# Kernel tuning notes

Hardware: AMD Instinct MI355X
Metric: run time of the kernel (lower is better)

Reference implementation:

```python
import jax, jax.numpy as jnp
import numpy as np

NEG_SLOPE = 0.2


def gat_layer(x, adj, W, a_src, a_dst):
    # x: (C, in_dim), adj: (C, C) 0/1, W: (in_dim, H*D), a_src/a_dst: (H, D)
    C = x.shape[0]
    H, D = a_src.shape
    h = (x @ W).reshape(C, H, D)            # (C, H, D)
    hh = jnp.transpose(h, (1, 0, 2))        # (H, C, D)
    asrc = jnp.einsum('hcd,hd->hc', hh, a_src)  # (H, C)
    adst = jnp.einsum('hcd,hd->hc', hh, a_dst)  # (H, C)
    e = asrc[:, :, None] + adst[:, None, :]     # (H, C, C)
    e = jax.nn.leaky_relu(e, NEG_SLOPE)
    e = jnp.where(adj[None, :, :] == 0, -jnp.inf, e)
    attn = jax.nn.softmax(e, axis=-1)           # (H, C, C)
    out = jnp.einsum('hij,hjd->hid', attn, hh)  # (H, C, D)
    return jnp.transpose(out, (1, 0, 2)).reshape(C, H * D)


def setup_inputs() -> dict:
    key = jax.random.key(0)
    ks = jax.random.split(key, 12)
    B, doc_dim = 1024, 768
    C, label_dim = 4096, 768
    hidden, H = 512, 4
    D = hidden // H  # 128

    doc_x = jax.random.normal(ks[0], (B, doc_dim), dtype=jnp.float32)
    label_init = jax.random.normal(ks[1], (C, label_dim), dtype=jnp.float32)
    adj = jax.random.randint(ks[2], (C, C), 0, 2, dtype=jnp.int32)
    adj = adj.at[jnp.arange(C), jnp.arange(C)].set(1)  # self-loops

    def xavier(k, shape):
        fan_in, fan_out = shape[0], shape[1]
        lim = jnp.sqrt(6.0 / (fan_in + fan_out)).astype(jnp.float32)
        return jax.random.uniform(k, shape, jnp.float32, -lim, lim)

    W1 = xavier(ks[3], (label_dim, hidden))
    a_src1 = xavier(ks[4], (H, D))
    a_dst1 = xavier(ks[5], (H, D))
    W2 = xavier(ks[6], (hidden, hidden))
    a_src2 = xavier(ks[7], (H, D))
    a_dst2 = xavier(ks[8], (H, D))
    Wd = xavier(ks[9], (doc_dim, hidden))
    bd = jnp.zeros((hidden,), jnp.float32)
    return {"doc_x": doc_x, "label_init": label_init, "adj": adj,
            "W1": W1, "a_src1": a_src1, "a_dst1": a_dst1,
            "W2": W2, "a_src2": a_src2, "a_dst2": a_dst2,
            "Wd": Wd, "bd": bd}


def reference(doc_x, label_init, adj, W1, a_src1, a_dst1, W2, a_src2, a_dst2, Wd, bd):
    # doc_proj (dropout = identity in eval)
    doc_h = jax.nn.relu(doc_x @ Wd + bd)            # (B, hidden)
    # label encoder: GAT -> ELU -> GAT
    h = gat_layer(label_init, adj, W1, a_src1, a_dst1)
    h = jax.nn.elu(h)
    label_h = gat_layer(h, adj, W2, a_src2, a_dst2)  # (C, hidden)
    logits = doc_h @ label_h.T                      # (B, C)
    return logits
```

## Files before the change

### kernel.cpp

```cpp
#include <hip/hip_runtime.h>
#include <hip/hip_bf16.h>
#include <math.h>

#define BDOCS   1024
#define CNODES  4096
#define INDIM   768
#define HID     512
#define NHEAD   4
#define HDIM    128
#define NEG_SLOPE 0.2f

#define KSPLIT  8
#define JPER    (CNODES / KSPLIT)
#define NCH     (JPER / 32)

typedef __attribute__((ext_vector_type(8))) short short8;
typedef __attribute__((ext_vector_type(4))) float f32x4;

__device__ __forceinline__ float lrelu(float x) { return x > 0.f ? x : NEG_SLOPE * x; }

__device__ __forceinline__ short f2bf(float f) {
    union { float f; unsigned u; } v; v.f = f;
    unsigned r = (v.u + 0x7fff + ((v.u >> 16) & 1)) >> 16;
    return (short)r;
}
__device__ __forceinline__ float bf2f(short s) {
    union { float f; unsigned u; } v; v.u = ((unsigned)(unsigned short)s) << 16;
    return v.f;
}
__device__ __forceinline__ unsigned pk2(float a, float b) {
    union { float f; unsigned u; } x, y; x.f = a; y.f = b;
    unsigned lo = (x.u + 0x7fff + ((x.u >> 16) & 1)) >> 16;
    unsigned hi = (y.u + 0x7fff + ((y.u >> 16) & 1)) >> 16;
    return lo | (hi << 16);
}
__device__ __forceinline__ short hup(float f) {
    union { float f; unsigned u; } v; v.f = f;
    return (short)((v.u + 0x8000) >> 16);
}
__device__ __forceinline__ unsigned encf(float x) {
    union { float f; unsigned u; } v; v.f = x;
    return (v.u & 0x80000000u) ? ~v.u : (v.u | 0x80000000u);
}
__device__ __forceinline__ float decf(unsigned u) {
    union { float f; unsigned u; } v;
    v.u = (u & 0x80000000u) ? (u ^ 0x80000000u) : ~u;
    return v.f;
}

__device__ void frag_T_dev(const float* __restrict__ src, short* __restrict__ dst,
                           int N, int K, int jc, int nq, float (*tile)[132])
{
    const int t  = threadIdx.x;
    const int KC = K >> 5;
#pragma unroll
    for (int it = 0; it < 16; it++) {
        const int e = it * 256 + t;
        const int j = e >> 7, n = e & 127;
        tile[j][n] = src[(size_t)(jc * 32 + j) * N + nq * 128 + n];
    }
    __syncthreads();
#pragma unroll
    for (int s = 0; s < 2; s++) {
        const int item = s * 256 + t;
        const int nbl = item >> 6, lane = item & 63;
        const int nr = lane & 15, kq = lane >> 4;
        short8 v;
#pragma unroll
        for (int jr = 0; jr < 8; jr++)
            v[jr] = f2bf(tile[kq * 8 + jr][nbl * 16 + nr]);
        *(short8*)&dst[((size_t)((nq * 8 + nbl) * KC + jc) * 64 + lane) * 8] = v;
    }
}

__device__ void frag_A_dev(const float* __restrict__ src, short* __restrict__ dst,
                           int C, int rb, int cq, float (*tile)[132])
{
    const int t  = threadIdx.x;
    const int KC = C >> 5;
#pragma unroll
    for (int it = 0; it < 8; it++) {
        const int e = it * 256 + t;
        const int r = e >> 7, c = e & 127;
        tile[r][c] = src[(size_t)(rb * 16 + r) * C + cq * 128 + c];
    }
    __syncthreads();
    const int kcl = t >> 6, lane = t & 63;
    const int m = lane & 15, kq = lane >> 4;
    short8 v8;
#pragma unroll
    for (int j = 0; j < 8; j++) v8[j] = f2bf(tile[m][kcl * 32 + kq * 8 + j]);
    *(short8*)&dst[((size_t)(rb * KC + cq * 4 + kcl) * 64 + lane) * 8] = v8;
}

#define PREP_BLOCKS (65536 + 96 + 96 + 64 + 384 + 1536)
__global__ __launch_bounds__(256)
void prep_all(const int* __restrict__ adj, unsigned long long* __restrict__ adjb64,
              const float* __restrict__ Wd, short* __restrict__ Wdf,
              const float* __restrict__ W1, short* __restrict__ W1f,
              const float* __restrict__ W2, short* __restrict__ W2f,
              const float* __restrict__ doc_x, short* __restrict__ dxf,
              const float* __restrict__ label_init, short* __restrict__ lif,
              unsigned* __restrict__ MhEnc)
{
    __shared__ float tile[32][132];
    int b = blockIdx.x;
    if (b < 65536) {
        if (b == 0 && threadIdx.x < 8) MhEnc[threadIdx.x] = 0u;
        const int t    = threadIdx.x;
        const int gw   = b * 4 + (t >> 6);
        const int lane = t & 63;
        const int i  = gw >> 6;
        const int j0 = (gw & 63) * 64;
        const int a  = adj[(size_t)i * CNODES + j0 + lane];
        const unsigned long long msk = __ballot(a != 0);
        if (lane == 0) adjb64[(size_t)i * 64 + (j0 >> 6)] = msk;
        return;
    }
    b -= 65536;
    if (b < 96)  { frag_T_dev(Wd, Wdf, HID, INDIM, b % 24, b / 24, tile); return; }
    b -= 96;
    if (b < 96)  { frag_T_dev(W1, W1f, HID, INDIM, b % 24, b / 24, tile); return; }
    b -= 96;
    if (b < 64)  { frag_T_dev(W2, W2f, HID, HID, b % 16, b / 16, tile); return; }
    b -= 64;
    if (b < 384) { frag_A_dev(doc_x, dxf, INDIM, b % 64, b / 64, tile); return; }
    b -= 384;
    frag_A_dev(label_init, lif, INDIM, b % 256, b / 256, tile);
}

template <int KC>
__global__ __launch_bounds__(64)
void gemm_hpre(const short* __restrict__ Af, const short* __restrict__ Bf,
               const float* __restrict__ a_src, const float* __restrict__ a_dst,
               short* __restrict__ hbTf, float* __restrict__ asrc, float* __restrict__ adst,
               unsigned* __restrict__ MhEnc)
{
    __shared__ __align__(16) short tileT[128][24];
    const int lane = threadIdx.x;
    const int mb   = blockIdx.x;
    const int nq   = blockIdx.y;
    const int i0   = mb * 16;

    f32x4 acc[8];
#pragma unroll
    for (int c = 0; c < 8; c++) acc[c] = (f32x4){0.f, 0.f, 0.f, 0.f};

    const short* ap = Af + (size_t)mb * KC * 512 + lane * 8;
    const short* bp = Bf + (size_t)(nq * 8) * KC * 512 + lane * 8;

#pragma unroll 2
    for (int kc = 0; kc < KC; kc++) {
        short8 a = *(const short8*)(ap + (size_t)kc * 512);
#pragma unroll
        for (int c = 0; c < 8; c++) {
            short8 bf = *(const short8*)(bp + ((size_t)c * KC + kc) * 512);
            acc[c] = __builtin_amdgcn_mfma_f32_16x16x32_bf16(a, bf, acc[c], 0, 0, 0);
        }
    }

    const int col = lane & 15, q4 = lane >> 4;

#pragma unroll
    for (int c = 0; c < 8; c++) {
        uint2 u;
        u.x = pk2(acc[c][0], acc[c][1]);
        u.y = pk2(acc[c][2], acc[c][3]);
        *(uint2*)&tileT[c * 16 + col][q4 * 4] = u;
    }
    __syncthreads();
    {
        const int jc = mb >> 1, khalf = mb & 1;
        const int nr = lane & 15, kq = lane >> 4;
        if ((kq >> 1) == khalf) {
#pragma unroll
            for (int nbl = 0; nbl < 8; nbl++) {
                short8 v = *(const short8*)&tileT[nbl * 16 + nr][(kq & 1) * 8];
                *(short8*)&hbTf[(((size_t)(nq * 8 + nbl) * (CNODES / 32) + jc) * 64 + lane) * 8] = v;
            }
        }
    }

    float ssrc[4] = {}, sdst[4] = {};
#pragma unroll
    for (int c = 0; c < 8; c++) {
        const float vs = a_src[nq * 128 + c * 16 + col];
        const float vd = a_dst[nq * 128 + c * 16 + col];
#pragma unroll
        for (int r = 0; r < 4; r++) {
            ssrc[r] += acc[c][r] * vs;
            sdst[r] += acc[c][r] * vd;
        }
    }
#pragma unroll
    for (int mask = 1; mask <= 8; mask <<= 1)
#pragma unroll
        for (int r = 0; r < 4; r++) {
            ssrc[r] += __shfl_xor(ssrc[r], mask);
            sdst[r] += __shfl_xor(sdst[r], mask);
        }
    if (col == 0) {
#pragma unroll
        for (int r = 0; r < 4; r++) {
            const int row = i0 + q4 * 4 + r;
            asrc[nq * CNODES + row] = ssrc[r];
            adst[nq * CNODES + row] = sdst[r];
        }
    }
    float wmax = fmaxf(fmaxf(sdst[0], sdst[1]), fmaxf(sdst[2], sdst[3]));
    wmax = fmaxf(wmax, __shfl_xor(wmax, 16));
    wmax = fmaxf(wmax, __shfl_xor(wmax, 32));
    if (lane == 0) atomicMax(MhEnc + nq, encf(wmax));
}

template <int KC>
__global__ __launch_bounds__(64)
void gemm_doc(const short* __restrict__ Af, const short* __restrict__ Bf,
              const float* __restrict__ bias, short* __restrict__ dhf)
{
    __shared__ __align__(16) short tile[16][64];
    const int lane = threadIdx.x;
    const int mb = blockIdx.x;
    const int ng = blockIdx.y;

    f32x4 acc[4];
#pragma unroll
    for (int c = 0; c < 4; c++) acc[c] = (f32x4){0.f, 0.f, 0.f, 0.f};

    const short* ap = Af + (size_t)mb * KC * 512 + lane * 8;
    const short* bp = Bf + (size_t)(ng * 4) * KC * 512 + lane * 8;

#pragma unroll 2
    for (int kc = 0; kc < KC; kc++) {
        short8 a = *(const short8*)(ap + (size_t)kc * 512);
#pragma unroll
        for (int c = 0; c < 4; c++) {
            short8 bf = *(const short8*)(bp + ((size_t)c * KC + kc) * 512);
            acc[c] = __builtin_amdgcn_mfma_f32_16x16x32_bf16(a, bf, acc[c], 0, 0, 0);
        }
    }

    const int col = lane & 15, q4 = lane >> 4;
#pragma unroll
    for (int c = 0; c < 4; c++)
#pragma unroll
        for (int r = 0; r < 4; r++) {
            float v = fmaxf(acc[c][r] + bias[ng * 64 + c * 16 + col], 0.f);
            tile[q4 * 4 + r][c * 16 + col] = f2bf(v);
        }
    __syncthreads();
    const int m = lane & 15, kq = lane >> 4;
#pragma unroll
    for (int kcl = 0; kcl < 2; kcl++) {
        short8 v = *(const short8*)&tile[m][kcl * 32 + kq * 8];
        *(short8*)&dhf[(((size_t)mb * 16 + ng * 2 + kcl) * 64 + lane) * 8] = v;
    }
}

template <int KC>
__global__ __launch_bounds__(64)
void gemm_frag(const short* __restrict__ Af, const short* __restrict__ Bf,
               float* __restrict__ Cmat, int N)
{
    const int lane = threadIdx.x;
    const int mb0  = blockIdx.x * 2;
    const int nq   = blockIdx.y;

    f32x4 acc[2][8];
#pragma unroll
    for (int f = 0; f < 2; f++)
#pragma unroll
        for (int c = 0; c < 8; c++) acc[f][c] = (f32x4){0.f, 0.f, 0.f, 0.f};

    const short* ap0 = Af + (size_t)mb0 * KC * 512 + lane * 8;
    const short* ap1 = ap0 + (size_t)KC * 512;
    const short* bp  = Bf + (size_t)(nq * 8) * KC * 512 + lane * 8;

#pragma unroll 2
    for (int kc = 0; kc < KC; kc++) {
        short8 a0 = *(const short8*)(ap0 + (size_t)kc * 512);
        short8 a1 = *(const short8*)(ap1 + (size_t)kc * 512);
#pragma unroll
        for (int c = 0; c < 8; c++) {
            short8 bf = *(const short8*)(bp + ((size_t)c * KC + kc) * 512);
            acc[0][c] = __builtin_amdgcn_mfma_f32_16x16x32_bf16(a0, bf, acc[0][c], 0, 0, 0);
            acc[1][c] = __builtin_amdgcn_mfma_f32_16x16x32_bf16(a1, bf, acc[1][c], 0, 0, 0);
        }
    }

    const int col = lane & 15, q4 = lane >> 4;
#pragma unroll
    for (int f = 0; f < 2; f++)
#pragma unroll
        for (int c = 0; c < 8; c++)
#pragma unroll
            for (int r = 0; r < 4; r++) {
                const int row = (mb0 + f) * 16 + q4 * 4 + r;
                Cmat[(size_t)row * N + nq * 128 + c * 16 + col] = acc[f][c][r];
            }
}

__global__ __launch_bounds__(512, 2)
void attn_pv(const short* __restrict__ hbTf,
             const unsigned int* __restrict__ adjb,
             const float* __restrict__ asrc, const float* __restrict__ adst,
             const unsigned* __restrict__ MhEnc,
             short* __restrict__ part, float* __restrict__ lpart)
{
    __shared__ __align__(16) float E1s[NHEAD][512];
    __shared__ __align__(16) float E2s[NHEAD][512];
    __shared__ __align__(16) short tileO[32][520];

    const int t    = threadIdx.x;
    const int ww   = t >> 6;
    const int w    = ww & 3;
    const int f2   = ww >> 2;
    const int lane = t & 63;
    const int m    = lane & 15;
    const int kq   = lane >> 4;
    const int i0   = blockIdx.x * 64;
    const int iw   = i0 + f2 * 32;
    const int ks   = blockIdx.y;
    const int js   = ks * JPER;

    {
        const int j = js + t;
#pragma unroll
        for (int h = 0; h < NHEAD; h++) {
            const float d = adst[h * CNODES + j] - decf(MhEnc[h]);
            E1s[h][t] = __expf(d);
            E2s[h][t] = __expf(0.2f * d);
        }
    }

    const float mh  = decf(MhEnc[w]);
    const float as0 = asrc[w * CNODES + iw + m];
    const float as1 = asrc[w * CNODES + iw + 16 + m];
    const float mr0 = lrelu(as0 + mh), mr1 = lrelu(as1 + mh);
    const float A10 = __expf(as0 + mh - mr0),          A11 = __expf(as1 + mh - mr1);
    const float A20 = __expf(0.2f * (as0 + mh) - mr0), A21 = __expf(0.2f * (as1 + mh) - mr1);
    const float T00 = __expf(-as0 - mh),               T01 = __expf(-as1 - mh);

    f32x4 acc[2][8], accO[2];
#pragma unroll
    for (int f = 0; f < 2; f++) {
        accO[f] = (f32x4){0.f, 0.f, 0.f, 0.f};
#pragma unroll
        for (int c = 0; c < 8; c++) acc[f][c] = (f32x4){0.f, 0.f, 0.f, 0.f};
    }
    short8 ones;
#pragma unroll
    for (int q = 0; q < 8; q++) ones[q] = (short)0x3F80;

    const unsigned int* ar0 = adjb + (size_t)(iw + m) * 128 + ks * NCH;
    const unsigned int* ar1 = adjb + (size_t)(iw + 16 + m) * 128 + ks * NCH;

    __syncthreads();

#pragma unroll 2
    for (int ch = 0; ch < NCH; ch++) {
        const int jl = ch * 32;
        const unsigned int aw0 = ar0[ch] >> (kq * 8);
        const unsigned int aw1 = ar1[ch] >> (kq * 8);
        const float4 x0 = *(const float4*)&E1s[w][jl + kq * 8];
        const float4 x1 = *(const float4*)&E1s[w][jl + kq * 8 + 4];
        const float4 y0 = *(const float4*)&E2s[w][jl + kq * 8];
        const float4 y1 = *(const float4*)&E2s[w][jl + kq * 8 + 4];
        const float e1v[8] = {x0.x, x0.y, x0.z, x0.w, x1.x, x1.y, x1.z, x1.w};
        const float e2v[8] = {y0.x, y0.y, y0.z, y0.w, y1.x, y1.y, y1.z, y1.w};

        short8 a0, a1;
#pragma unroll
        for (int q = 0; q < 8; q++) {
            const float e1 = e1v[q], e2 = e2v[q];
            const bool c0 = e1 > T00, c1 = e1 > T01;
            float w0 = (c0 ? A10 : A20) * (c0 ? e1 : e2);
            float w1 = (c1 ? A11 : A21) * (c1 ? e1 : e2);
            w0 = ((aw0 >> q) & 1u) ? w0 : 0.f;
            w1 = ((aw1 >> q) & 1u) ? w1 : 0.f;
            a0[q] = hup(w0);
            a1[q] = hup(w1);
        }

        const short* bbase = hbTf + (((size_t)(w * 8) * 128 + ((js + jl) >> 5)) * 64 + lane) * 8;
#pragma unroll
        for (int c = 0; c < 8; c++) {
            short8 bf = *(const short8*)(bbase + (size_t)c * 128 * 64 * 8);
            acc[0][c] = __builtin_amdgcn_mfma_f32_16x16x32_bf16(a0, bf, acc[0][c], 0, 0, 0);
            acc[1][c] = __builtin_amdgcn_mfma_f32_16x16x32_bf16(a1, bf, acc[1][c], 0, 0, 0);
        }
        accO[0] = __builtin_amdgcn_mfma_f32_16x16x32_bf16(a0, ones, accO[0], 0, 0, 0);
        accO[1] = __builtin_amdgcn_mfma_f32_16x16x32_bf16(a1, ones, accO[1], 0, 0, 0);
    }

    if (m == 0) {
#pragma unroll
        for (int f = 0; f < 2; f++)
#pragma unroll
            for (int r = 0; r < 4; r++)
                lpart[((size_t)ks * NHEAD + w) * CNODES + iw + f * 16 + kq * 4 + r] = accO[f][r];
    }

    short* pS = part + (size_t)ks * CNODES * HID;
    for (int half = 0; half < 2; half++) {
        __syncthreads();
        if (f2 == half) {
#pragma unroll
            for (int f = 0; f < 2; f++)
#pragma unroll
                for (int c = 0; c < 8; c++)
#pragma unroll
                    for (int r = 0; r < 4; r++)
                        tileO[f * 16 + kq * 4 + r][w * 128 + c * 16 + m] = f2bf(acc[f][c][r]);
        }
        __syncthreads();
#pragma unroll
        for (int it = 0; it < 4; it++) {
            const int u   = it * 512 + t;
            const int row = u >> 6, un = u & 63;
            uint4 v = *(const uint4*)&tileO[row][un * 8];
            *(uint4*)&pS[(size_t)(i0 + half * 32 + row) * HID + un * 8] = v;
        }
    }
}

template <bool ELU>
__global__ __launch_bounds__(256)
void reduce_norm_frag(const short* __restrict__ part, const float* __restrict__ lpart,
                      short* __restrict__ dst)
{
    const int t = threadIdx.x;
    const int W = blockIdx.x * 4 + (t >> 6);
    const int lane = t & 63;
    const int rb = W >> 4, kc = W & 15;
    const int m = lane & 15, kq = lane >> 4;
    const int i = rb * 16 + m;
    const int n0 = kc * 32 + kq * 8;
    const int h = kc >> 2;

    float v[8] = {};
    float l = 0.f;
#pragma unroll
    for (int s = 0; s < KSPLIT; s++) {
        const uint4 raw = *(const uint4*)&part[(size_t)s * CNODES * HID + (size_t)i * HID + n0];
        const unsigned rr[4] = {raw.x, raw.y, raw.z, raw.w};
#pragma unroll
        for (int q = 0; q < 4; q++) {
            v[q * 2]     += bf2f((short)(rr[q] & 0xffff));
            v[q * 2 + 1] += bf2f((short)(rr[q] >> 16));
        }
        l += lpart[((size_t)s * NHEAD + h) * CNODES + i];
    }
    const float inv = 1.0f / l;
    short8 o;
#pragma unroll
    for (int q = 0; q < 8; q++) {
        float x = v[q] * inv;
        if (ELU) x = x > 0.f ? x : (__expf(x) - 1.f);
        o[q] = f2bf(x);
    }
    *(short8*)&dst[((size_t)(rb * 16 + kc) * 64 + lane) * 8] = o;
}

extern "C" void kernel_launch(void* const* d_in, const int* in_sizes, int n_in,
                              void* d_out, int out_size, void* d_ws, size_t ws_size,
                              hipStream_t stream)
{
    const float* doc_x      = (const float*)d_in[0];
    const float* label_init = (const float*)d_in[1];
    const int*   adj        = (const int*)d_in[2];
    const float* W1         = (const float*)d_in[3];
    const float* a_src1     = (const float*)d_in[4];
    const float* a_dst1     = (const float*)d_in[5];
    const float* W2         = (const float*)d_in[6];
    const float* a_src2     = (const float*)d_in[7];
    const float* a_dst2     = (const float*)d_in[8];
    const float* Wd         = (const float*)d_in[9];
    const float* bd         = (const float*)d_in[10];
    float*       out        = (float*)d_out;

    char* wsb = (char*)d_ws;
    size_t off = 0;
    auto alloc = [&](size_t bytes) -> char* {
        char* p = wsb + off;
        off = (off + bytes + 255) & ~(size_t)255;
        return p;
    };

    float* asrc  = (float*)alloc(NHEAD * CNODES * 4);
    float* adst  = (float*)alloc(NHEAD * CNODES * 4);
    unsigned* MhEnc = (unsigned*)alloc(256);
    float* lpart = (float*)alloc((size_t)KSPLIT * NHEAD * CNODES * 4);
    unsigned int* adjb = (unsigned int*)alloc((size_t)CNODES * 128 * 4);
    short* hbTf  = (short*)alloc((size_t)CNODES * HID * 2);
    short* Wdf   = (short*)alloc((size_t)INDIM * HID * 2);
    short* W1f   = (short*)alloc((size_t)INDIM * HID * 2);
    short* W2f   = (short*)alloc((size_t)HID * HID * 2);
    short* dxf   = (short*)alloc((size_t)BDOCS * INDIM * 2);
    short* Af_li = (short*)alloc((size_t)CNODES * INDIM * 2);
    short* Af2   = (short*)alloc((size_t)CNODES * HID * 2);
    short* lhf   = (short*)alloc((size_t)CNODES * HID * 2);
    short* dhf   = (short*)alloc((size_t)BDOCS * HID * 2);
    short* part  = (short*)alloc((size_t)KSPLIT * CNODES * HID * 2);
    (void)ws_size;

    const dim3 blk(256);

    prep_all<<<PREP_BLOCKS, blk, 0, stream>>>(adj, (unsigned long long*)adjb,
                                              Wd, Wdf, W1, W1f, W2, W2f,
                                              doc_x, dxf, label_init, Af_li, MhEnc);

    gemm_doc<INDIM / 32><<<dim3(BDOCS / 16, HID / 64), 64, 0, stream>>>(dxf, Wdf, bd, dhf);

    gemm_hpre<INDIM / 32><<<dim3(CNODES / 16, NHEAD), 64, 0, stream>>>(
        Af_li, W1f, a_src1, a_dst1, hbTf, asrc, adst, MhEnc);

    attn_pv<<<dim3(CNODES / 64, KSPLIT), 512, 0, stream>>>(
        hbTf, adjb, asrc, adst, MhEnc, part, lpart);
    reduce_norm_frag<true><<<CNODES * HID / 256 / 8, blk, 0, stream>>>(part, lpart, Af2);

    gemm_hpre<HID / 32><<<dim3(CNODES / 16, NHEAD), 64, 0, stream>>>(
        Af2, W2f, a_src2, a_dst2, hbTf, asrc, adst, MhEnc + 4);

    attn_pv<<<dim3(CNODES / 64, KSPLIT), 512, 0, stream>>>(
        hbTf, adjb, asrc, adst, MhEnc + 4, part, lpart);
    reduce_norm_frag<false><<<CNODES * HID / 256 / 8, blk, 0, stream>>>(part, lpart, lhf);

    gemm_frag<HID / 32><<<dim3(BDOCS / 32, CNODES / 128), 64, 0, stream>>>(dhf, lhf, out, CNODES);
}
```

Before: 394.1 us.

## Halve GEMM output tile width to double block counts across projection kernels

Each 64-thread block of the head-projection, doc-projection and final logits GEMMs now covers half as many output columns, so each grid has twice as many blocks and the small GEMMs spread across more compute units. For the head projection, each head's 128 columns are split over two blocks. Their partial attention scores are combined with float atomicAdd into buffers zeroed by added memsets. The per-head max is kept as two partial maxima that are summed, which gives an upper bound used as the softmax shift. The cost is extra atomics, two memset launches, repeated A-operand loads, and a looser shift that could reduce precision in the exponentials.

```diff
diff --git a/kernel.cpp b/kernel.cpp
--- a/kernel.cpp
+++ b/kernel.cpp
@@ -106,7 +106,7 @@
     __shared__ float tile[32][132];
     int b = blockIdx.x;
     if (b < 65536) {
-        if (b == 0 && threadIdx.x < 8) MhEnc[threadIdx.x] = 0u;
+        if (b == 0 && threadIdx.x < 16) MhEnc[threadIdx.x] = 0x007FFFFFu;
         const int t    = threadIdx.x;
         const int gw   = b * 4 + (t >> 6);
         const int lane = t & 63;
@@ -134,26 +134,27 @@
 void gemm_hpre(const short* __restrict__ Af, const short* __restrict__ Bf,
                const float* __restrict__ a_src, const float* __restrict__ a_dst,
                short* __restrict__ hbTf, float* __restrict__ asrc, float* __restrict__ adst,
-               unsigned* __restrict__ MhEnc)
-{
-    __shared__ __align__(16) short tileT[128][24];
+               unsigned* __restrict__ MhEncH)
+{
+    __shared__ __align__(16) short tileT[64][24];
     const int lane = threadIdx.x;
     const int mb   = blockIdx.x;
-    const int nq   = blockIdx.y;
+    const int h    = blockIdx.y >> 1;
+    const int ch   = blockIdx.y & 1;
     const int i0   = mb * 16;
 
-    f32x4 acc[8];
-#pragma unroll
-    for (int c = 0; c < 8; c++) acc[c] = (f32x4){0.f, 0.f, 0.f, 0.f};
+    f32x4 acc[4];
+#pragma unroll
+    for (int c = 0; c < 4; c++) acc[c] = (f32x4){0.f, 0.f, 0.f, 0.f};
 
     const short* ap = Af + (size_t)mb * KC * 512 + lane * 8;
-    const short* bp = Bf + (size_t)(nq * 8) * KC * 512 + lane * 8;
+    const short* bp = Bf + (size_t)(h * 8 + ch * 4) * KC * 512 + lane * 8;
 
 #pragma unroll 2
     for (int kc = 0; kc < KC; kc++) {
         short8 a = *(const short8*)(ap + (size_t)kc * 512);
 #pragma unroll
-        for (int c = 0; c < 8; c++) {
+        for (int c = 0; c < 4; c++) {
             short8 bf = *(const short8*)(bp + ((size_t)c * KC + kc) * 512);
             acc[c] = __builtin_amdgcn_mfma_f32_16x16x32_bf16(a, bf, acc[c], 0, 0, 0);
         }
@@ -162,7 +163,7 @@
     const int col = lane & 15, q4 = lane >> 4;
 
 #pragma unroll
-    for (int c = 0; c < 8; c++) {
+    for (int c = 0; c < 4; c++) {
         uint2 u;
         u.x = pk2(acc[c][0], acc[c][1]);
         u.y = pk2(acc[c][2], acc[c][3]);
@@ -174,18 +175,19 @@
         const int nr = lane & 15, kq = lane >> 4;
         if ((kq >> 1) == khalf) {
 #pragma unroll
-            for (int nbl = 0; nbl < 8; nbl++) {
-                short8 v = *(const short8*)&tileT[nbl * 16 + nr][(kq & 1) * 8];
-                *(short8*)&hbTf[(((size_t)(nq * 8 + nbl) * (CNODES / 32) + jc) * 64 + lane) * 8] = v;
+            for (int cl = 0; cl < 4; cl++) {
+                short8 v = *(const short8*)&tileT[cl * 16 + nr][(kq & 1) * 8];
+                const int nbl = h * 8 + ch * 4 + cl;
+                *(short8*)&hbTf[(((size_t)nbl * (CNODES / 32) + jc) * 64 + lane) * 8] = v;
             }
         }
     }
 
     float ssrc[4] = {}, sdst[4] = {};
 #pragma unroll
-    for (int c = 0; c < 8; c++) {
-        const float vs = a_src[nq * 128 + c * 16 + col];
-        const float vd = a_dst[nq * 128 + c * 16 + col];
+    for (int c = 0; c < 4; c++) {
+        const float vs = a_src[h * 128 + ch * 64 + c * 16 + col];
+        const float vd = a_dst[h * 128 + ch * 64 + c * 16 + col];
 #pragma unroll
         for (int r = 0; r < 4; r++) {
             ssrc[r] += acc[c][r] * vs;
@@ -203,14 +205,14 @@
 #pragma unroll
         for (int r = 0; r < 4; r++) {
             const int row = i0 + q4 * 4 + r;
-            asrc[nq * CNODES + row] = ssrc[r];
-            adst[nq * CNODES + row] = sdst[r];
+            atomicAdd(asrc + h * CNODES + row, ssrc[r]);
+            atomicAdd(adst + h * CNODES + row, sdst[r]);
         }
     }
     float wmax = fmaxf(fmaxf(sdst[0], sdst[1]), fmaxf(sdst[2], sdst[3]));
     wmax = fmaxf(wmax, __shfl_xor(wmax, 16));
     wmax = fmaxf(wmax, __shfl_xor(wmax, 32));
-    if (lane == 0) atomicMax(MhEnc + nq, encf(wmax));
+    if (lane == 0) atomicMax(MhEncH + h * 2 + ch, encf(wmax));
 }
 
 template <int KC>
@@ -218,23 +220,23 @@
 void gemm_doc(const short* __restrict__ Af, const short* __restrict__ Bf,
               const float* __restrict__ bias, short* __restrict__ dhf)
 {
-    __shared__ __align__(16) short tile[16][64];
+    __shared__ __align__(16) short tile[16][32];
     const int lane = threadIdx.x;
     const int mb = blockIdx.x;
     const int ng = blockIdx.y;
 
-    f32x4 acc[4];
-#pragma unroll
-    for (int c = 0; c < 4; c++) acc[c] = (f32x4){0.f, 0.f, 0.f, 0.f};
+    f32x4 acc[2];
+#pragma unroll
+    for (int c = 0; c < 2; c++) acc[c] = (f32x4){0.f, 0.f, 0.f, 0.f};
 
     const short* ap = Af + (size_t)mb * KC * 512 + lane * 8;
-    const short* bp = Bf + (size_t)(ng * 4) * KC * 512 + lane * 8;
+    const short* bp = Bf + (size_t)(ng * 2) * KC * 512 + lane * 8;
 
 #pragma unroll 2
     for (int kc = 0; kc < KC; kc++) {
         short8 a = *(const short8*)(ap + (size_t)kc * 512);
 #pragma unroll
-        for (int c = 0; c < 4; c++) {
+        for (int c = 0; c < 2; c++) {
             short8 bf = *(const short8*)(bp + ((size_t)c * KC + kc) * 512);
             acc[c] = __builtin_amdgcn_mfma_f32_16x16x32_bf16(a, bf, acc[c], 0, 0, 0);
         }
@@ -242,19 +244,16 @@
 
     const int col = lane & 15, q4 = lane >> 4;
 #pragma unroll
-    for (int c = 0; c < 4; c++)
+    for (int c = 0; c < 2; c++)
 #pragma unroll
         for (int r = 0; r < 4; r++) {
-            float v = fmaxf(acc[c][r] + bias[ng * 64 + c * 16 + col], 0.f);
+            float v = fmaxf(acc[c][r] + bias[ng * 32 + c * 16 + col], 0.f);
             tile[q4 * 4 + r][c * 16 + col] = f2bf(v);
         }
     __syncthreads();
     const int m = lane & 15, kq = lane >> 4;
-#pragma unroll
-    for (int kcl = 0; kcl < 2; kcl++) {
-        short8 v = *(const short8*)&tile[m][kcl * 32 + kq * 8];
-        *(short8*)&dhf[(((size_t)mb * 16 + ng * 2 + kcl) * 64 + lane) * 8] = v;
-    }
+    short8 v = *(const short8*)&tile[m][kq * 8];
+    *(short8*)&dhf[(((size_t)mb * 16 + ng) * 64 + lane) * 8] = v;
 }
 
 template <int KC>
@@ -264,24 +263,24 @@
 {
     const int lane = threadIdx.x;
     const int mb0  = blockIdx.x * 2;
-    const int nq   = blockIdx.y;
-
-    f32x4 acc[2][8];
+    const int ng   = blockIdx.y;
+
+    f32x4 acc[2][4];
 #pragma unroll
     for (int f = 0; f < 2; f++)
 #pragma unroll
-        for (int c = 0; c < 8; c++) acc[f][c] = (f32x4){0.f, 0.f, 0.f, 0.f};
+        for (int c = 0; c < 4; c++) acc[f][c] = (f32x4){0.f, 0.f, 0.f, 0.f};
 
     const short* ap0 = Af + (size_t)mb0 * KC * 512 + lane * 8;
     const short* ap1 = ap0 + (size_t)KC * 512;
-    const short* bp  = Bf + (size_t)(nq * 8) * KC * 512 + lane * 8;
+    const short* bp  = Bf + (size_t)(ng * 4) * KC * 512 + lane * 8;
 
 #pragma unroll 2
     for (int kc = 0; kc < KC; kc++) {
         short8 a0 = *(const short8*)(ap0 + (size_t)kc * 512);
         short8 a1 = *(const short8*)(ap1 + (size_t)kc * 512);
 #pragma unroll
-        for (int c = 0; c < 8; c++) {
+        for (int c = 0; c < 4; c++) {
             short8 bf = *(const short8*)(bp + ((size_t)c * KC + kc) * 512);
             acc[0][c] = __builtin_amdgcn_mfma_f32_16x16x32_bf16(a0, bf, acc[0][c], 0, 0, 0);
             acc[1][c] = __builtin_amdgcn_mfma_f32_16x16x32_bf16(a1, bf, acc[1][c], 0, 0, 0);
@@ -292,11 +291,11 @@
 #pragma unroll
     for (int f = 0; f < 2; f++)
 #pragma unroll
-        for (int c = 0; c < 8; c++)
+        for (int c = 0; c < 4; c++)
 #pragma unroll
             for (int r = 0; r < 4; r++) {
                 const int row = (mb0 + f) * 16 + q4 * 4 + r;
-                Cmat[(size_t)row * N + nq * 128 + c * 16 + col] = acc[f][c][r];
+                Cmat[(size_t)row * N + ng * 64 + c * 16 + col] = acc[f][c][r];
             }
 }
 
@@ -304,7 +303,7 @@
 void attn_pv(const short* __restrict__ hbTf,
              const unsigned int* __restrict__ adjb,
              const float* __restrict__ asrc, const float* __restrict__ adst,
-             const unsigned* __restrict__ MhEnc,
+             const unsigned* __restrict__ MhEncH,
              short* __restrict__ part, float* __restrict__ lpart)
 {
     __shared__ __align__(16) float E1s[NHEAD][512];
@@ -327,13 +326,14 @@
         const int j = js + t;
 #pragma unroll
         for (int h = 0; h < NHEAD; h++) {
-            const float d = adst[h * CNODES + j] - decf(MhEnc[h]);
+            const float mhh = decf(MhEncH[h * 2]) + decf(MhEncH[h * 2 + 1]);
+            const float d = adst[h * CNODES + j] - mhh;
             E1s[h][t] = __expf(d);
             E2s[h][t] = __expf(0.2f * d);
         }
     }
 
-    const float mh  = decf(MhEnc[w]);
+    const float mh  = decf(MhEncH[w * 2]) + decf(MhEncH[w * 2 + 1]);
     const float as0 = asrc[w * CNODES + iw + m];
     const float as1 = asrc[w * CNODES + iw + 16 + m];
     const float mr0 = lrelu(as0 + mh), mr1 = lrelu(as1 + mh);
@@ -489,7 +489,7 @@
 
     float* asrc  = (float*)alloc(NHEAD * CNODES * 4);
     float* adst  = (float*)alloc(NHEAD * CNODES * 4);
-    unsigned* MhEnc = (unsigned*)alloc(256);
+    unsigned* MhEncH = (unsigned*)alloc(256);
     float* lpart = (float*)alloc((size_t)KSPLIT * NHEAD * CNODES * 4);
     unsigned int* adjb = (unsigned int*)alloc((size_t)CNODES * 128 * 4);
     short* hbTf  = (short*)alloc((size_t)CNODES * HID * 2);
@@ -506,25 +506,29 @@
 
     const dim3 blk(256);
 
+    hipMemsetAsync(asrc, 0, (size_t)2 * NHEAD * CNODES * 4, stream);
+
     prep_all<<<PREP_BLOCKS, blk, 0, stream>>>(adj, (unsigned long long*)adjb,
                                               Wd, Wdf, W1, W1f, W2, W2f,
-                                              doc_x, dxf, label_init, Af_li, MhEnc);
-
-    gemm_doc<INDIM / 32><<<dim3(BDOCS / 16, HID / 64), 64, 0, stream>>>(dxf, Wdf, bd, dhf);
-
-    gemm_hpre<INDIM / 32><<<dim3(CNODES / 16, NHEAD), 64, 0, stream>>>(
-        Af_li, W1f, a_src1, a_dst1, hbTf, asrc, adst, MhEnc);
+                                              doc_x, dxf, label_init, Af_li, MhEncH);
+
+    gemm_doc<INDIM / 32><<<dim3(BDOCS / 16, HID / 32), 64, 0, stream>>>(dxf, Wdf, bd, dhf);
+
+    gemm_hpre<INDIM / 32><<<dim3(CNODES / 16, 2 * NHEAD), 64, 0, stream>>>(
+        Af_li, W1f, a_src1, a_dst1, hbTf, asrc, adst, MhEncH);
 
     attn_pv<<<dim3(CNODES / 64, KSPLIT), 512, 0, stream>>>(
-        hbTf, adjb, asrc, adst, MhEnc, part, lpart);
+        hbTf, adjb, asrc, adst, MhEncH, part, lpart);
     reduce_norm_frag<true><<<CNODES * HID / 256 / 8, blk, 0, stream>>>(part, lpart, Af2);
 
-    gemm_hpre<HID / 32><<<dim3(CNODES / 16, NHEAD), 64, 0, stream>>>(
-        Af2, W2f, a_src2, a_dst2, hbTf, asrc, adst, MhEnc + 4);
+    hipMemsetAsync(asrc, 0, (size_t)2 * NHEAD * CNODES * 4, stream);
+
+    gemm_hpre<HID / 32><<<dim3(CNODES / 16, 2 * NHEAD), 64, 0, stream>>>(
+        Af2, W2f, a_src2, a_dst2, hbTf, asrc, adst, MhEncH + 8);
 
     attn_pv<<<dim3(CNODES / 64, KSPLIT), 512, 0, stream>>>(
-        hbTf, adjb, asrc, adst, MhEnc + 4, part, lpart);
+        hbTf, adjb, asrc, adst, MhEncH + 8, part, lpart);
     reduce_norm_frag<false><<<CNODES * HID / 256 / 8, blk, 0, stream>>>(part, lpart, lhf);
 
-    gemm_frag<HID / 32><<<dim3(BDOCS / 32, CNODES / 128), 64, 0, stream>>>(dhf, lhf, out, CNODES);
-}
+    gemm_frag<HID / 32><<<dim3(BDOCS / 32, CNODES / 64), 64, 0, stream>>>(dhf, lhf, out, CNODES);
+}
```

Result: faster. 357.4 us (-9.3%).
